# Optimization experiments

Measured on AMD Instinct MI355X. Metric: run time of the kernel, lower is better.

The kernel has to match this reference:

```python
import jax, jax.numpy as jnp
import numpy as np

N_NODES = 50000
N_EDGES = 800000
NUM_FEATURES = 128
HIDDEN = 256
OUT = 64


def setup_inputs() -> dict:
    key = jax.random.key(0)
    k1, k2, k3, k4 = jax.random.split(key, 4)
    x = jax.random.normal(k1, (N_NODES, NUM_FEATURES), dtype=jnp.float32)
    # Glorot-ish scaled weights
    W1 = jax.random.normal(k2, (NUM_FEATURES, HIDDEN), dtype=jnp.float32) * (1.0 / np.sqrt(NUM_FEATURES))
    b1 = jnp.zeros((HIDDEN,), dtype=jnp.float32)
    W2 = jax.random.normal(k3, (HIDDEN, OUT), dtype=jnp.float32) * (1.0 / np.sqrt(HIDDEN))
    b2 = jnp.zeros((OUT,), dtype=jnp.float32)
    edge_index = jax.random.randint(k4, (2, N_EDGES), 0, N_NODES, dtype=jnp.int64)
    return {"x": x, "W1": W1, "b1": b1, "W2": W2, "b2": b2,
            "edge_index": edge_index, "batch_size": 2, "pred_steps": 12}


def _gcn_conv(x, W, b, row, col, n):
    """PyG-style GCNConv: x' = D^-1/2 (A + I) D^-1/2 (x W) + b.
    row/col already include self-loops."""
    deg = jax.ops.segment_sum(jnp.ones_like(row, dtype=x.dtype), row, num_segments=n)
    dinv = jnp.where(deg > 0, deg ** -0.5, 0.0)
    norm = dinv[row] * dinv[col]          # [E+N]
    h = x @ W                              # transform first (in < out irrelevant here)
    msg = h[col] * norm[:, None]           # gather + scale: [E+N, d_out]
    agg = jax.ops.segment_sum(msg, row, num_segments=n)  # scatter-add
    return agg + b


def reference(x, W1, b1, W2, b2, edge_index, batch_size, pred_steps):
    n = x.shape[0]
    loops = jnp.arange(n, dtype=edge_index.dtype)
    row = jnp.concatenate([edge_index[0], loops])  # add self-loops once, reused by both convs
    col = jnp.concatenate([edge_index[1], loops])

    h = jax.nn.relu(_gcn_conv(x, W1, b1, row, col, n))
    # F.dropout in eval mode is identity (inference baseline)
    h = _gcn_conv(h, W2, b2, row, col, n)
    h = jax.nn.log_softmax(h, axis=1)      # [N, OUT]
    # unsqueeze/expand/repeat -> [batch_size, pred_steps, N, OUT]
    out = jnp.broadcast_to(h[None, None, :, :], (batch_size, pred_steps, n, h.shape[1]))
    return out
```

## Files before the change

### kernel.cpp

```cpp
#include <hip/hip_runtime.h>

__global__ __launch_bounds__(256) void hist_rows(const int* __restrict__ row, int* __restrict__ cnt, int E) {
    int e = blockIdx.x * 256 + threadIdx.x;
    if (e < E) atomicAdd(&cnt[row[e]], 1);
}

__global__ __launch_bounds__(256) void alloc_buckets(const int* __restrict__ cnt,
                                                     int* __restrict__ base, int* __restrict__ fill,
                                                     float* __restrict__ dinv,
                                                     int* __restrict__ total, int n) {
    int i = blockIdx.x * 256 + threadIdx.x;
    if (i >= n) return;
    int c = cnt[i];
    int cp = (c + 7) & ~7;
    int b = atomicAdd(total, cp);
    base[i] = b;
    fill[i] = b;
    dinv[i] = rsqrtf(1.0f + (float)c);
}

__global__ __launch_bounds__(256) void fill_buckets(const int* __restrict__ row, const int* __restrict__ col,
                                                    int* __restrict__ fill, const float* __restrict__ dinv,
                                                    int2* __restrict__ edge2, int E) {
    int e = blockIdx.x * 256 + threadIdx.x;
    if (e < E) {
        int r = row[e], c = col[e];
        int pos = atomicAdd(&fill[r], 1);
        edge2[pos] = make_int2(c, __float_as_int(dinv[r] * dinv[c]));
    }
}

__global__ __launch_bounds__(256) void agg_x(const float* __restrict__ x,
                                             const int* __restrict__ base, const int* __restrict__ cnt,
                                             const int2* __restrict__ edge2, const float* __restrict__ dinv,
                                             float* __restrict__ AGGX, int n) {
    int w = (blockIdx.x * 256 + threadIdx.x) >> 6;
    int lane = threadIdx.x & 63;
    if (w >= n) return;
    float di = dinv[w];
    float2 xv = ((const float2*)(x + (size_t)w * 128))[lane];
    float2 a0 = make_float2(xv.x * di * di, xv.y * di * di);
    float2 a1 = make_float2(0.f, 0.f), a2 = a1, a3 = a1;
    const int2* eb = edge2 + base[w];
    int dp = (cnt[w] + 7) & ~7;
    for (int j = 0; j < dp; j += 8) {
        int2 e[8];
        #pragma unroll
        for (int u = 0; u < 8; ++u) e[u] = eb[j + u];
        float2 v[8];
        #pragma unroll
        for (int u = 0; u < 8; ++u)
            v[u] = ((const float2*)(x + (size_t)e[u].x * 128))[lane];
        #pragma unroll
        for (int u = 0; u < 8; ++u) {
            float nr = __int_as_float(e[u].y);
            float2* a = (u & 3) == 0 ? &a0 : (u & 3) == 1 ? &a1 : (u & 3) == 2 ? &a2 : &a3;
            a->x = fmaf(v[u].x, nr, a->x);
            a->y = fmaf(v[u].y, nr, a->y);
        }
    }
    float2 o = make_float2(a0.x + a1.x + a2.x + a3.x, a0.y + a1.y + a2.y + a3.y);
    ((float2*)(AGGX + (size_t)w * 128))[lane] = o;
}

__global__ __launch_bounds__(256) void agg_h2(const float* __restrict__ H2,
                                              const int* __restrict__ base, const int* __restrict__ cnt,
                                              const int2* __restrict__ edge2, const float* __restrict__ dinv,
                                              const float* __restrict__ b2,
                                              float* __restrict__ AGG2, int n) {
    int w = (blockIdx.x * 256 + threadIdx.x) >> 6;
    int lane = threadIdx.x & 63;
    if (w >= n) return;
    float di = dinv[w];
    float a0 = H2[(size_t)w * 64 + lane] * di * di;
    float a1 = 0.f, a2 = 0.f, a3 = 0.f;
    const int2* eb = edge2 + base[w];
    int dp = (cnt[w] + 7) & ~7;
    for (int j = 0; j < dp; j += 8) {
        int2 e[8];
        #pragma unroll
        for (int u = 0; u < 8; ++u) e[u] = eb[j + u];
        float v[8];
        #pragma unroll
        for (int u = 0; u < 8; ++u)
            v[u] = H2[(size_t)e[u].x * 64 + lane];
        #pragma unroll
        for (int u = 0; u < 8; ++u) {
            float nr = __int_as_float(e[u].y);
            float* a = (u & 3) == 0 ? &a0 : (u & 3) == 1 ? &a1 : (u & 3) == 2 ? &a2 : &a3;
            *a = fmaf(v[u], nr, *a);
        }
    }
    AGG2[(size_t)w * 64 + lane] = a0 + a1 + a2 + a3 + b2[lane];
}

__global__ __launch_bounds__(256) void gemm64(const float* __restrict__ A,
                                              const float* __restrict__ B,
                                              const float* __restrict__ bias,
                                              float* __restrict__ C,
                                              int M, int N, int K, int relu) {
    __shared__ float As[32][68];
    __shared__ float Bs[32][68];
    const int bm = blockIdx.x * 64;
    const int bn = blockIdx.y * 64;
    const int tid = threadIdx.x;
    const int tx = tid & 15;
    const int ty = tid >> 4;
    float acc[4][4] = {};

    for (int k0 = 0; k0 < K; k0 += 32) {
        #pragma unroll
        for (int i = 0; i < 8; ++i) {
            int t = tid + i * 256;
            int r = t >> 5, c = t & 31;
            int gr = bm + r;
            float v = 0.f;
            if (gr < M) v = A[(size_t)gr * K + k0 + c];
            As[c][r] = v;
        }
        #pragma unroll
        for (int i = 0; i < 8; ++i) {
            int t = tid + i * 256;
            int r = t >> 6, c = t & 63;
            Bs[r][c] = B[(size_t)(k0 + r) * N + bn + c];
        }
        __syncthreads();
        #pragma unroll
        for (int k = 0; k < 32; ++k) {
            float4 av = *(const float4*)&As[k][ty * 4];
            float4 bv = *(const float4*)&Bs[k][tx * 4];
            float a4[4] = {av.x, av.y, av.z, av.w};
            float b4[4] = {bv.x, bv.y, bv.z, bv.w};
            #pragma unroll
            for (int i2 = 0; i2 < 4; ++i2)
                #pragma unroll
                for (int j = 0; j < 4; ++j)
                    acc[i2][j] = fmaf(a4[i2], b4[j], acc[i2][j]);
        }
        __syncthreads();
    }
    float bv4[4];
    #pragma unroll
    for (int j = 0; j < 4; ++j) bv4[j] = bias ? bias[bn + tx * 4 + j] : 0.f;
    #pragma unroll
    for (int i2 = 0; i2 < 4; ++i2) {
        int gr = bm + ty * 4 + i2;
        if (gr < M) {
            float4 o;
            o.x = acc[i2][0] + bv4[0];
            o.y = acc[i2][1] + bv4[1];
            o.z = acc[i2][2] + bv4[2];
            o.w = acc[i2][3] + bv4[3];
            if (relu) {
                o.x = fmaxf(o.x, 0.f); o.y = fmaxf(o.y, 0.f);
                o.z = fmaxf(o.z, 0.f); o.w = fmaxf(o.w, 0.f);
            }
            *(float4*)(C + (size_t)gr * N + bn + tx * 4) = o;
        }
    }
}

__global__ __launch_bounds__(256) void final_out(const float* __restrict__ AGG2,
                                                 float* __restrict__ out, int n, int copies) {
    int w = (blockIdx.x * 256 + threadIdx.x) >> 6;
    int lane = threadIdx.x & 63;
    if (w >= n) return;
    size_t idx = (size_t)w * 64 + lane;
    float v = AGG2[idx];
    float m = v;
    #pragma unroll
    for (int off = 32; off > 0; off >>= 1) m = fmaxf(m, __shfl_xor(m, off, 64));
    float e = expf(v - m);
    float s = e;
    #pragma unroll
    for (int off = 32; off > 0; off >>= 1) s += __shfl_xor(s, off, 64);
    float res = v - m - logf(s);
    size_t stride = (size_t)n * 64;
    for (int c = 0; c < copies; ++c) out[(size_t)c * stride + idx] = res;
}

extern "C" void kernel_launch(void* const* d_in, const int* in_sizes, int n_in,
                              void* d_out, int out_size, void* d_ws, size_t ws_size,
                              hipStream_t stream) {
    const float* x  = (const float*)d_in[0];
    const float* W1 = (const float*)d_in[1];
    const float* b1 = (const float*)d_in[2];
    const float* W2 = (const float*)d_in[3];
    const float* b2 = (const float*)d_in[4];
    const int*   ei = (const int*)d_in[5];

    const int n = in_sizes[0] / 128;
    const int E = in_sizes[5] / 2;
    float* out = (float*)d_out;
    const size_t stride = (size_t)n * 64;
    const int copies = (int)(out_size / stride);

    float* dinv  = out;
    int*   cnt   = (int*)(out + n);
    int*   base  = (int*)(out + 2 * (size_t)n);
    int*   fill  = (int*)(out + 3 * (size_t)n);
    int*   total = (int*)(out + 4 * (size_t)n);
    int2*  edge2 = (int2*)(out + 1 * stride);
    float* AGGX  = out + 2 * stride;
    float* H1    = out + 4 * stride;
    float* H2    = out + 8 * stride;
    float* AGG2  = out + 9 * stride;

    hipMemsetAsync(cnt, 0, (3 * (size_t)n + 64) * sizeof(int), stream);
    hipMemsetAsync(edge2, 0, ((size_t)E + 8 * (size_t)n) * sizeof(int2), stream);

    hist_rows    <<<(E + 255) / 256, 256, 0, stream>>>(ei, cnt, E);
    alloc_buckets<<<(n + 255) / 256, 256, 0, stream>>>(cnt, base, fill, dinv, total, n);
    fill_buckets <<<(E + 255) / 256, 256, 0, stream>>>(ei, ei + E, fill, dinv, edge2, E);

    agg_x<<<(n + 3) / 4, 256, 0, stream>>>(x, base, cnt, edge2, dinv, AGGX, n);
    gemm64<<<dim3((n + 63) / 64, 4), 256, 0, stream>>>(AGGX, W1, b1, H1, n, 256, 128, 1);

    gemm64<<<dim3((n + 63) / 64, 1), 256, 0, stream>>>(H1, W2, nullptr, H2, n, 64, 256, 0);
    agg_h2<<<(n + 3) / 4, 256, 0, stream>>>(H2, base, cnt, edge2, dinv, b2, AGG2, n);

    final_out<<<(n + 3) / 4, 256, 0, stream>>>(AGG2, out, n, copies);
}
```

Before: 606.2 us.

## Use split-bf16 MFMA GEMMs, prefetch edge lists, drop memset, add nontemporal stores

Both dense GEMMs move from FP32 FMA tiles to bf16 MFMA instructions, with each operand split into high and low bf16 parts and three products summed to keep near-FP32 accuracy. The block order is remapped across XCDs. The aggregation kernels prefetch the next batch of 8 edges while gathering the current one. The full-edge-buffer memset is replaced by zeroing only the padding slots inside alloc_buckets. Nontemporal loads and stores are added to streaming outputs. The 3-pass split adds MFMA work and shared-memory traffic, and precision could drift slightly.

```diff
diff --git a/kernel.cpp b/kernel.cpp
--- a/kernel.cpp
+++ b/kernel.cpp
@@ -1,4 +1,17 @@
 #include <hip/hip_runtime.h>
+
+typedef float  f32x2  __attribute__((ext_vector_type(2)));
+typedef float  f32x4  __attribute__((ext_vector_type(4)));
+typedef __bf16 bf16x8 __attribute__((ext_vector_type(8)));
+
+static __device__ __forceinline__ void split_pair(float a, float b, unsigned& hp, unsigned& lp) {
+    __bf16 ha = (__bf16)a, hb = (__bf16)b;
+    hp = (unsigned)__builtin_bit_cast(unsigned short, ha) |
+         ((unsigned)__builtin_bit_cast(unsigned short, hb) << 16);
+    __bf16 la = (__bf16)(a - (float)ha), lb = (__bf16)(b - (float)hb);
+    lp = (unsigned)__builtin_bit_cast(unsigned short, la) |
+         ((unsigned)__builtin_bit_cast(unsigned short, lb) << 16);
+}
 
 __global__ __launch_bounds__(256) void hist_rows(const int* __restrict__ row, int* __restrict__ cnt, int E) {
     int e = blockIdx.x * 256 + threadIdx.x;
@@ -8,7 +21,8 @@
 __global__ __launch_bounds__(256) void alloc_buckets(const int* __restrict__ cnt,
                                                      int* __restrict__ base, int* __restrict__ fill,
                                                      float* __restrict__ dinv,
-                                                     int* __restrict__ total, int n) {
+                                                     int* __restrict__ total,
+                                                     int2* __restrict__ edge2, int n) {
     int i = blockIdx.x * 256 + threadIdx.x;
     if (i >= n) return;
     int c = cnt[i];
@@ -17,6 +31,7 @@
     base[i] = b;
     fill[i] = b;
     dinv[i] = rsqrtf(1.0f + (float)c);
+    for (int p = b + c; p < b + cp; ++p) edge2[p] = make_int2(0, 0);
 }
 
 __global__ __launch_bounds__(256) void fill_buckets(const int* __restrict__ row, const int* __restrict__ col,
@@ -38,29 +53,48 @@
     int lane = threadIdx.x & 63;
     if (w >= n) return;
     float di = dinv[w];
-    float2 xv = ((const float2*)(x + (size_t)w * 128))[lane];
-    float2 a0 = make_float2(xv.x * di * di, xv.y * di * di);
-    float2 a1 = make_float2(0.f, 0.f), a2 = a1, a3 = a1;
+    f32x2 xv = ((const f32x2*)(x + (size_t)w * 128))[lane];
+    f32x2 a0 = xv * (di * di);
+    f32x2 a1 = {0.f, 0.f}, a2 = {0.f, 0.f}, a3 = {0.f, 0.f};
     const int2* eb = edge2 + base[w];
     int dp = (cnt[w] + 7) & ~7;
-    for (int j = 0; j < dp; j += 8) {
+    if (dp > 0) {
         int2 e[8];
         #pragma unroll
-        for (int u = 0; u < 8; ++u) e[u] = eb[j + u];
-        float2 v[8];
-        #pragma unroll
-        for (int u = 0; u < 8; ++u)
-            v[u] = ((const float2*)(x + (size_t)e[u].x * 128))[lane];
-        #pragma unroll
-        for (int u = 0; u < 8; ++u) {
-            float nr = __int_as_float(e[u].y);
-            float2* a = (u & 3) == 0 ? &a0 : (u & 3) == 1 ? &a1 : (u & 3) == 2 ? &a2 : &a3;
-            a->x = fmaf(v[u].x, nr, a->x);
-            a->y = fmaf(v[u].y, nr, a->y);
-        }
-    }
-    float2 o = make_float2(a0.x + a1.x + a2.x + a3.x, a0.y + a1.y + a2.y + a3.y);
-    ((float2*)(AGGX + (size_t)w * 128))[lane] = o;
+        for (int u = 0; u < 8; ++u) e[u] = eb[u];
+        int j = 0;
+        for (; j + 8 < dp; j += 8) {
+            f32x2 v[8];
+            #pragma unroll
+            for (int u = 0; u < 8; ++u)
+                v[u] = ((const f32x2*)(x + (size_t)e[u].x * 128))[lane];
+            int2 en[8];
+            #pragma unroll
+            for (int u = 0; u < 8; ++u) en[u] = eb[j + 8 + u];
+            #pragma unroll
+            for (int u = 0; u < 8; ++u) {
+                float nr = __int_as_float(e[u].y);
+                f32x2* a = (u & 3) == 0 ? &a0 : (u & 3) == 1 ? &a1 : (u & 3) == 2 ? &a2 : &a3;
+                *a += v[u] * nr;
+            }
+            #pragma unroll
+            for (int u = 0; u < 8; ++u) e[u] = en[u];
+        }
+        {
+            f32x2 v[8];
+            #pragma unroll
+            for (int u = 0; u < 8; ++u)
+                v[u] = ((const f32x2*)(x + (size_t)e[u].x * 128))[lane];
+            #pragma unroll
+            for (int u = 0; u < 8; ++u) {
+                float nr = __int_as_float(e[u].y);
+                f32x2* a = (u & 3) == 0 ? &a0 : (u & 3) == 1 ? &a1 : (u & 3) == 2 ? &a2 : &a3;
+                *a += v[u] * nr;
+            }
+        }
+    }
+    f32x2 o = a0 + a1 + a2 + a3;
+    __builtin_nontemporal_store(o, (f32x2*)(AGGX + (size_t)w * 128) + lane);
 }
 
 __global__ __launch_bounds__(256) void agg_h2(const float* __restrict__ H2,
@@ -76,86 +110,139 @@
     float a1 = 0.f, a2 = 0.f, a3 = 0.f;
     const int2* eb = edge2 + base[w];
     int dp = (cnt[w] + 7) & ~7;
-    for (int j = 0; j < dp; j += 8) {
+    if (dp > 0) {
         int2 e[8];
         #pragma unroll
-        for (int u = 0; u < 8; ++u) e[u] = eb[j + u];
-        float v[8];
-        #pragma unroll
-        for (int u = 0; u < 8; ++u)
-            v[u] = H2[(size_t)e[u].x * 64 + lane];
-        #pragma unroll
-        for (int u = 0; u < 8; ++u) {
-            float nr = __int_as_float(e[u].y);
-            float* a = (u & 3) == 0 ? &a0 : (u & 3) == 1 ? &a1 : (u & 3) == 2 ? &a2 : &a3;
-            *a = fmaf(v[u], nr, *a);
-        }
-    }
-    AGG2[(size_t)w * 64 + lane] = a0 + a1 + a2 + a3 + b2[lane];
-}
-
-__global__ __launch_bounds__(256) void gemm64(const float* __restrict__ A,
-                                              const float* __restrict__ B,
-                                              const float* __restrict__ bias,
-                                              float* __restrict__ C,
-                                              int M, int N, int K, int relu) {
-    __shared__ float As[32][68];
-    __shared__ float Bs[32][68];
-    const int bm = blockIdx.x * 64;
-    const int bn = blockIdx.y * 64;
-    const int tid = threadIdx.x;
-    const int tx = tid & 15;
-    const int ty = tid >> 4;
-    float acc[4][4] = {};
+        for (int u = 0; u < 8; ++u) e[u] = eb[u];
+        int j = 0;
+        for (; j + 8 < dp; j += 8) {
+            float v[8];
+            #pragma unroll
+            for (int u = 0; u < 8; ++u)
+                v[u] = H2[(size_t)e[u].x * 64 + lane];
+            int2 en[8];
+            #pragma unroll
+            for (int u = 0; u < 8; ++u) en[u] = eb[j + 8 + u];
+            #pragma unroll
+            for (int u = 0; u < 8; ++u) {
+                float nr = __int_as_float(e[u].y);
+                float* a = (u & 3) == 0 ? &a0 : (u & 3) == 1 ? &a1 : (u & 3) == 2 ? &a2 : &a3;
+                *a = fmaf(v[u], nr, *a);
+            }
+            #pragma unroll
+            for (int u = 0; u < 8; ++u) e[u] = en[u];
+        }
+        {
+            float v[8];
+            #pragma unroll
+            for (int u = 0; u < 8; ++u)
+                v[u] = H2[(size_t)e[u].x * 64 + lane];
+            #pragma unroll
+            for (int u = 0; u < 8; ++u) {
+                float nr = __int_as_float(e[u].y);
+                float* a = (u & 3) == 0 ? &a0 : (u & 3) == 1 ? &a1 : (u & 3) == 2 ? &a2 : &a3;
+                *a = fmaf(v[u], nr, *a);
+            }
+        }
+    }
+    float o = a0 + a1 + a2 + a3 + b2[lane];
+    __builtin_nontemporal_store(o, AGG2 + (size_t)w * 64 + lane);
+}
+
+template<int NT_IN, int NT_OUT>
+__global__ __launch_bounds__(256) void gemm_mfma(const float* __restrict__ A,
+                                                 const float* __restrict__ B,
+                                                 const float* __restrict__ bias,
+                                                 float* __restrict__ C,
+                                                 int M, int N, int K, int relu) {
+    __shared__ unsigned Ah[4][64][4], Al[4][64][4], Bh[4][64][4], Bl[4][64][4];
+
+    const int nbn = gridDim.x;
+    const int nl  = (nbn == 4) ? 2 : 0;
+    const int tot = nbn * gridDim.y;
+    int flat = blockIdx.x + nbn * blockIdx.y;
+    int q = tot >> 3, r = tot & 7;
+    int x8 = flat & 7, i8 = flat >> 3;
+    int f2 = (x8 < r ? x8 * (q + 1) : r * (q + 1) + (x8 - r) * q) + i8;
+    const int bn = (f2 & (nbn - 1)) * 64;
+    const int bm = (f2 >> nl) * 64;
+
+    const int tid  = threadIdx.x;
+    const int lane = tid & 63;
+    const int wv   = tid >> 6;
+    const int wr   = wv >> 1, wc = wv & 1;
+    const int lg   = lane >> 4, lr = lane & 15;
+
+    f32x4 acc[2][2] = {};
 
     for (int k0 = 0; k0 < K; k0 += 32) {
         #pragma unroll
-        for (int i = 0; i < 8; ++i) {
-            int t = tid + i * 256;
-            int r = t >> 5, c = t & 31;
-            int gr = bm + r;
-            float v = 0.f;
-            if (gr < M) v = A[(size_t)gr * K + k0 + c];
-            As[c][r] = v;
-        }
-        #pragma unroll
-        for (int i = 0; i < 8; ++i) {
-            int t = tid + i * 256;
-            int r = t >> 6, c = t & 63;
-            Bs[r][c] = B[(size_t)(k0 + r) * N + bn + c];
+        for (int i = 0; i < 4; ++i) {
+            int t  = tid + i * 256;
+            int rr = t >> 4;
+            int kp = t & 15;
+            int gr = bm + rr;
+            f32x2 v = {0.f, 0.f};
+            if (gr < M) {
+                const f32x2* p = (const f32x2*)(A + (size_t)gr * K + k0 + 2 * kp);
+                v = NT_IN ? __builtin_nontemporal_load(p) : *p;
+            }
+            unsigned hp, lp;
+            split_pair(v.x, v.y, hp, lp);
+            Ah[kp >> 2][rr][kp & 3] = hp;
+            Al[kp >> 2][rr][kp & 3] = lp;
+        }
+        #pragma unroll
+        for (int i = 0; i < 4; ++i) {
+            int t  = tid + i * 256;
+            int cc = t & 63;
+            int kp = t >> 6;
+            const float* p = B + (size_t)(k0 + 2 * kp) * N + bn + cc;
+            float v0 = p[0], v1 = p[N];
+            unsigned hp, lp;
+            split_pair(v0, v1, hp, lp);
+            Bh[kp >> 2][cc][kp & 3] = hp;
+            Bl[kp >> 2][cc][kp & 3] = lp;
         }
         __syncthreads();
-        #pragma unroll
-        for (int k = 0; k < 32; ++k) {
-            float4 av = *(const float4*)&As[k][ty * 4];
-            float4 bv = *(const float4*)&Bs[k][tx * 4];
-            float a4[4] = {av.x, av.y, av.z, av.w};
-            float b4[4] = {bv.x, bv.y, bv.z, bv.w};
-            #pragma unroll
-            for (int i2 = 0; i2 < 4; ++i2)
-                #pragma unroll
-                for (int j = 0; j < 4; ++j)
-                    acc[i2][j] = fmaf(a4[i2], b4[j], acc[i2][j]);
-        }
+
+        bf16x8 ah[2], al[2], bh[2], bl[2];
+        #pragma unroll
+        for (int f = 0; f < 2; ++f) {
+            int ar = wr * 32 + f * 16 + lr;
+            ah[f] = *(const bf16x8*)&Ah[lg][ar][0];
+            al[f] = *(const bf16x8*)&Al[lg][ar][0];
+            int bc = wc * 32 + f * 16 + lr;
+            bh[f] = *(const bf16x8*)&Bh[lg][bc][0];
+            bl[f] = *(const bf16x8*)&Bl[lg][bc][0];
+        }
+        #pragma unroll
+        for (int fi = 0; fi < 2; ++fi)
+            #pragma unroll
+            for (int fj = 0; fj < 2; ++fj) {
+                acc[fi][fj] = __builtin_amdgcn_mfma_f32_16x16x32_bf16(ah[fi], bh[fj], acc[fi][fj], 0, 0, 0);
+                acc[fi][fj] = __builtin_amdgcn_mfma_f32_16x16x32_bf16(ah[fi], bl[fj], acc[fi][fj], 0, 0, 0);
+                acc[fi][fj] = __builtin_amdgcn_mfma_f32_16x16x32_bf16(al[fi], bh[fj], acc[fi][fj], 0, 0, 0);
+            }
         __syncthreads();
     }
-    float bv4[4];
+
     #pragma unroll
-    for (int j = 0; j < 4; ++j) bv4[j] = bias ? bias[bn + tx * 4 + j] : 0.f;
-    #pragma unroll
-    for (int i2 = 0; i2 < 4; ++i2) {
-        int gr = bm + ty * 4 + i2;
-        if (gr < M) {
-            float4 o;
-            o.x = acc[i2][0] + bv4[0];
-            o.y = acc[i2][1] + bv4[1];
-            o.z = acc[i2][2] + bv4[2];
-            o.w = acc[i2][3] + bv4[3];
-            if (relu) {
-                o.x = fmaxf(o.x, 0.f); o.y = fmaxf(o.y, 0.f);
-                o.z = fmaxf(o.z, 0.f); o.w = fmaxf(o.w, 0.f);
-            }
-            *(float4*)(C + (size_t)gr * N + bn + tx * 4) = o;
+    for (int fj = 0; fj < 2; ++fj) {
+        int col = bn + wc * 32 + fj * 16 + lr;
+        float bv = bias ? bias[col] : 0.f;
+        #pragma unroll
+        for (int fi = 0; fi < 2; ++fi) {
+            #pragma unroll
+            for (int rg = 0; rg < 4; ++rg) {
+                int gr = bm + wr * 32 + fi * 16 + lg * 4 + rg;
+                if (gr < M) {
+                    float o = acc[fi][fj][rg] + bv;
+                    if (relu) o = fmaxf(o, 0.f);
+                    if (NT_OUT) __builtin_nontemporal_store(o, C + (size_t)gr * N + col);
+                    else        C[(size_t)gr * N + col] = o;
+                }
+            }
         }
     }
 }
@@ -166,7 +253,7 @@
     int lane = threadIdx.x & 63;
     if (w >= n) return;
     size_t idx = (size_t)w * 64 + lane;
-    float v = AGG2[idx];
+    float v = __builtin_nontemporal_load(AGG2 + idx);
     float m = v;
     #pragma unroll
     for (int off = 32; off > 0; off >>= 1) m = fmaxf(m, __shfl_xor(m, off, 64));
@@ -176,7 +263,8 @@
     for (int off = 32; off > 0; off >>= 1) s += __shfl_xor(s, off, 64);
     float res = v - m - logf(s);
     size_t stride = (size_t)n * 64;
-    for (int c = 0; c < copies; ++c) out[(size_t)c * stride + idx] = res;
+    for (int c = 0; c < copies; ++c)
+        __builtin_nontemporal_store(res, out + (size_t)c * stride + idx);
 }
 
 extern "C" void kernel_launch(void* const* d_in, const int* in_sizes, int n_in,
@@ -207,16 +295,15 @@
     float* AGG2  = out + 9 * stride;
 
     hipMemsetAsync(cnt, 0, (3 * (size_t)n + 64) * sizeof(int), stream);
-    hipMemsetAsync(edge2, 0, ((size_t)E + 8 * (size_t)n) * sizeof(int2), stream);
 
     hist_rows    <<<(E + 255) / 256, 256, 0, stream>>>(ei, cnt, E);
-    alloc_buckets<<<(n + 255) / 256, 256, 0, stream>>>(cnt, base, fill, dinv, total, n);
+    alloc_buckets<<<(n + 255) / 256, 256, 0, stream>>>(cnt, base, fill, dinv, total, edge2, n);
     fill_buckets <<<(E + 255) / 256, 256, 0, stream>>>(ei, ei + E, fill, dinv, edge2, E);
 
     agg_x<<<(n + 3) / 4, 256, 0, stream>>>(x, base, cnt, edge2, dinv, AGGX, n);
-    gemm64<<<dim3((n + 63) / 64, 4), 256, 0, stream>>>(AGGX, W1, b1, H1, n, 256, 128, 1);
-
-    gemm64<<<dim3((n + 63) / 64, 1), 256, 0, stream>>>(H1, W2, nullptr, H2, n, 64, 256, 0);
+    gemm_mfma<0, 1><<<dim3(4, (n + 63) / 64), 256, 0, stream>>>(AGGX, W1, b1, H1, n, 256, 128, 1);
+
+    gemm_mfma<1, 0><<<dim3(1, (n + 63) / 64), 256, 0, stream>>>(H1, W2, nullptr, H2, n, 64, 256, 0);
     agg_h2<<<(n + 3) / 4, 256, 0, stream>>>(H2, base, cnt, edge2, dinv, b2, AGG2, n);
 
     final_out<<<(n + 3) / 4, 256, 0, stream>>>(AGG2, out, n, copies);
```

Measured after the change: 596.4 us. Within noise of the previous version (-1.6%).
